# Kernel optimization log

Hardware: AMD Instinct MI355X
Metric: run time of the kernel (lower is better)

Reference implementation:

```python
import jax, jax.numpy as jnp
import numpy as np

IN_DIM, HID, OUT_DIM = 128, 24, 4096
B, K = 16384, 256

def setup_inputs() -> dict:
    key = jax.random.key(0)
    ks = jax.random.split(key, 8)
    x = jax.random.normal(ks[0], (B, IN_DIM), dtype=jnp.float32)
    possible_moves = jax.random.randint(ks[1], (B, K), 0, OUT_DIM)
    s1 = 1.0 / np.sqrt(IN_DIM)
    s2 = 1.0 / np.sqrt(HID)
    W1 = jax.random.uniform(ks[2], (IN_DIM, HID), jnp.float32, -s1, s1)
    b1 = jax.random.uniform(ks[3], (HID,), jnp.float32, -s1, s1)
    W2 = jax.random.uniform(ks[4], (HID, HID), jnp.float32, -s2, s2)
    b2 = jax.random.uniform(ks[5], (HID,), jnp.float32, -s2, s2)
    W3 = jax.random.uniform(ks[6], (HID, OUT_DIM), jnp.float32, -s2, s2)
    b3 = jax.random.uniform(ks[7], (OUT_DIM,), jnp.float32, -s2, s2)
    return {"x": x, "possible_moves": possible_moves,
            "W1": W1, "b1": b1, "W2": W2, "b2": b2, "W3": W3, "b3": b3}

def reference(x, possible_moves, W1, b1, W2, b2, W3, b3):
    # small MLP: 128 -> 24 -> 24 -> 4096
    h = jax.nn.relu(x @ W1 + b1)
    h = jax.nn.relu(h @ W2 + b2)
    logits = h @ W3 + b3                     # [B, OUT_DIM]
    # per-row legal-move mask via vectorized scatter (duplicates just re-set 1)
    Bn = logits.shape[0]
    rows = jnp.arange(Bn)[:, None]           # [B, 1] broadcasts over K
    mask = jnp.zeros_like(logits).at[rows, possible_moves].set(1.0)
    # faithful to original: multiply (not -inf) then softmax over full dim
    filtered = logits * mask
    return jax.nn.softmax(filtered, axis=1)
```

## Files before the change

### kernel.cpp

```cpp
#include <hip/hip_runtime.h>
#include <hip/hip_bf16.h>

#define IN_DIM 128
#define HID 24
#define OUT_DIM 4096
#define NB 16384
#define KMOV 256

#define TR_BLOCKS 384
#define MLP_BLOCKS (NB / 8)

__global__ __launch_bounds__(256) void kprep(const float* __restrict__ x,
                                             const float* __restrict__ W1,
                                             const float* __restrict__ b1,
                                             const float* __restrict__ W2,
                                             const float* __restrict__ b2,
                                             const float* __restrict__ W3,
                                             float* __restrict__ W3T,
                                             float* __restrict__ h2out) {
    __shared__ float W1s[IN_DIM * HID];
    __shared__ float W2s[HID * HID];
    __shared__ float b1s[HID], b2s[HID];
    __shared__ float xs[8][IN_DIM];

    int bid = blockIdx.x;
    int t = threadIdx.x;

    if (bid < TR_BLOCKS) {
        int i = bid * 256 + t;
        int c = i / HID;
        int k = i - c * HID;
        W3T[i] = W3[k * OUT_DIM + c];
        return;
    }

    for (int i = t; i < IN_DIM * HID; i += 256) W1s[i] = W1[i];
    for (int i = t; i < HID * HID; i += 256)    W2s[i] = W2[i];
    if (t < HID) { b1s[t] = b1[t]; b2s[t] = b2[t]; }
    int rbase = (bid - TR_BLOCKS) * 8;
    for (int i = t; i < 8 * IN_DIM; i += 256)
        xs[i >> 7][i & 127] = x[(size_t)rbase * IN_DIM + i];
    __syncthreads();

    int g = t >> 5;
    int j = t & 31;
    int r = rbase + g;

    float h1 = 0.f;
    if (j < HID) {
        h1 = b1s[j];
        #pragma unroll 8
        for (int i = 0; i < IN_DIM; i++) h1 += xs[g][i] * W1s[i * HID + j];
        h1 = fmaxf(h1, 0.f);
    }
    float h2 = (j < HID) ? b2s[j] : 0.f;
    #pragma unroll
    for (int k = 0; k < HID; k++) {
        float hk = __shfl(h1, k, 32);
        if (j < HID) h2 += hk * W2s[k * HID + j];
    }
    if (j < HID) {
        h2 = fmaxf(h2, 0.f);
        h2out[(size_t)r * HID + j] = h2;
    }
}

__global__ __launch_bounds__(256) void kmain(const int* __restrict__ moves,
                                             const float* __restrict__ b3,
                                             const float* __restrict__ W3T,
                                             const float* __restrict__ h2all,
                                             float* __restrict__ out) {
    __shared__ unsigned char claimed[OUT_DIM];
    __shared__ float h2s[HID];
    __shared__ float red[8];

    int r = blockIdx.x;
    int t = threadIdx.x;

    int c = moves[(size_t)r * KMOV + t];
    if (t < HID) h2s[t] = h2all[(size_t)r * HID + t];
    __syncthreads();

    const float4* w = (const float4*)(W3T + c * HID);
    float4 a0 = w[0], a1 = w[1], a2 = w[2], a3 = w[3], a4 = w[4], a5 = w[5];
    float acc = b3[c];
    acc += a0.x*h2s[0] + a0.y*h2s[1] + a0.z*h2s[2]  + a0.w*h2s[3];
    acc += a1.x*h2s[4] + a1.y*h2s[5] + a1.z*h2s[6]  + a1.w*h2s[7];
    acc += a2.x*h2s[8] + a2.y*h2s[9] + a2.z*h2s[10] + a2.w*h2s[11];
    acc += a3.x*h2s[12]+ a3.y*h2s[13]+ a3.z*h2s[14] + a3.w*h2s[15];
    acc += a4.x*h2s[16]+ a4.y*h2s[17]+ a4.z*h2s[18] + a4.w*h2s[19];
    acc += a5.x*h2s[20]+ a5.y*h2s[21]+ a5.z*h2s[22] + a5.w*h2s[23];

    claimed[c] = (unsigned char)t;

    float m = acc;
    #pragma unroll
    for (int off = 32; off > 0; off >>= 1) m = fmaxf(m, __shfl_xor(m, off, 64));
    int wid = t >> 6;
    if ((t & 63) == 0) red[wid] = m;
    __syncthreads();
    float mm = fmaxf(fmaxf(fmaxf(red[0], red[1]), fmaxf(red[2], red[3])), 0.f);

    float e      = __expf(acc - mm);
    float base_e = __expf(-mm);

    float contrib = (claimed[c] == (unsigned char)t) ? (e - base_e) : 0.f;
    float s = contrib;
    #pragma unroll
    for (int off = 32; off > 0; off >>= 1) s += __shfl_xor(s, off, 64);
    if ((t & 63) == 0) red[4 + wid] = s;
    __syncthreads();
    float denom = (float)OUT_DIM * base_e + (red[4] + red[5] + red[6] + red[7]);
    float inv = 1.0f / denom;
    float oc  = base_e * inv;

    float4 ocv = make_float4(oc, oc, oc, oc);
    float4* out4 = (float4*)(out + (size_t)r * OUT_DIM);
    #pragma unroll
    for (int i = 0; i < 4; i++) out4[t + i * 256] = ocv;

    __syncthreads();

    out[(size_t)r * OUT_DIM + c] = e * inv;
}

extern "C" void kernel_launch(void* const* d_in, const int* in_sizes, int n_in,
                              void* d_out, int out_size, void* d_ws, size_t ws_size,
                              hipStream_t stream) {
    const float* x     = (const float*)d_in[0];
    const int*   moves = (const int*)  d_in[1];
    const float* W1    = (const float*)d_in[2];
    const float* b1    = (const float*)d_in[3];
    const float* W2    = (const float*)d_in[4];
    const float* b2    = (const float*)d_in[5];
    const float* W3    = (const float*)d_in[6];
    const float* b3    = (const float*)d_in[7];
    float* out = (float*)d_out;

    float* W3T = (float*)d_ws;
    float* h2  = (float*)((char*)d_ws + OUT_DIM * HID * 4);

    kprep<<<TR_BLOCKS + MLP_BLOCKS, 256, 0, stream>>>(x, W1, b1, W2, b2, W3, W3T, h2);
    kmain<<<NB, 256, 0, stream>>>(moves, b3, W3T, h2, out);
}
```

Baseline: 343.0 us.

## Fuse per-row MLP into main softmax kernel, split W3 transpose into own kernel

Moves the two-layer MLP computation into the per-row main kernel so each block computes its own hidden vector, removing the h2 round trip through global memory. The W3 transpose becomes a tiny separate kernel. In exchange, every one of the 16384 blocks reloads W1 (12 KB) and W2 into shared memory and runs the 128x24 dot products serially on a single wavefront, which adds latency and L2 traffic per block.

```diff
diff --git a/kernel.cpp b/kernel.cpp
--- a/kernel.cpp
+++ b/kernel.cpp
@@ -7,78 +7,61 @@
 #define NB 16384
 #define KMOV 256
 
-#define TR_BLOCKS 384
-#define MLP_BLOCKS (NB / 8)
+__global__ __launch_bounds__(256) void ktr(const float* __restrict__ W3,
+                                           float* __restrict__ W3T) {
+    int i = blockIdx.x * 256 + threadIdx.x;
+    int c = i / HID;
+    int k = i - c * HID;
+    W3T[i] = W3[k * OUT_DIM + c];
+}
 
-__global__ __launch_bounds__(256) void kprep(const float* __restrict__ x,
-                                             const float* __restrict__ W1,
-                                             const float* __restrict__ b1,
-                                             const float* __restrict__ W2,
-                                             const float* __restrict__ b2,
-                                             const float* __restrict__ W3,
-                                             float* __restrict__ W3T,
-                                             float* __restrict__ h2out) {
+__global__ __launch_bounds__(256) void kfused(const float* __restrict__ x,
+                                              const float* __restrict__ W1,
+                                              const float* __restrict__ b1,
+                                              const float* __restrict__ W2,
+                                              const float* __restrict__ b2,
+                                              const float* __restrict__ b3,
+                                              const float* __restrict__ W3T,
+                                              const int* __restrict__ moves,
+                                              float* __restrict__ out) {
     __shared__ float W1s[IN_DIM * HID];
     __shared__ float W2s[HID * HID];
-    __shared__ float b1s[HID], b2s[HID];
-    __shared__ float xs[8][IN_DIM];
-
-    int bid = blockIdx.x;
-    int t = threadIdx.x;
-
-    if (bid < TR_BLOCKS) {
-        int i = bid * 256 + t;
-        int c = i / HID;
-        int k = i - c * HID;
-        W3T[i] = W3[k * OUT_DIM + c];
-        return;
-    }
-
-    for (int i = t; i < IN_DIM * HID; i += 256) W1s[i] = W1[i];
-    for (int i = t; i < HID * HID; i += 256)    W2s[i] = W2[i];
-    if (t < HID) { b1s[t] = b1[t]; b2s[t] = b2[t]; }
-    int rbase = (bid - TR_BLOCKS) * 8;
-    for (int i = t; i < 8 * IN_DIM; i += 256)
-        xs[i >> 7][i & 127] = x[(size_t)rbase * IN_DIM + i];
-    __syncthreads();
-
-    int g = t >> 5;
-    int j = t & 31;
-    int r = rbase + g;
-
-    float h1 = 0.f;
-    if (j < HID) {
-        h1 = b1s[j];
-        #pragma unroll 8
-        for (int i = 0; i < IN_DIM; i++) h1 += xs[g][i] * W1s[i * HID + j];
-        h1 = fmaxf(h1, 0.f);
-    }
-    float h2 = (j < HID) ? b2s[j] : 0.f;
-    #pragma unroll
-    for (int k = 0; k < HID; k++) {
-        float hk = __shfl(h1, k, 32);
-        if (j < HID) h2 += hk * W2s[k * HID + j];
-    }
-    if (j < HID) {
-        h2 = fmaxf(h2, 0.f);
-        h2out[(size_t)r * HID + j] = h2;
-    }
-}
-
-__global__ __launch_bounds__(256) void kmain(const int* __restrict__ moves,
-                                             const float* __restrict__ b3,
-                                             const float* __restrict__ W3T,
-                                             const float* __restrict__ h2all,
-                                             float* __restrict__ out) {
+    __shared__ float xs[IN_DIM];
+    __shared__ float b1s[HID], b2s[HID], h2s[HID];
     __shared__ unsigned char claimed[OUT_DIM];
-    __shared__ float h2s[HID];
     __shared__ float red[8];
 
     int r = blockIdx.x;
     int t = threadIdx.x;
 
+    {
+        float4* W1v = (float4*)W1s;
+        const float4* W1g = (const float4*)W1;
+        #pragma unroll
+        for (int i = 0; i < 3; i++) W1v[t + i * 256] = W1g[t + i * 256];
+        if (t < 144) ((float4*)W2s)[t] = ((const float4*)W2)[t];
+        if (t < IN_DIM) xs[t] = x[(size_t)r * IN_DIM + t];
+        if (t < HID) { b1s[t] = b1[t]; b2s[t] = b2[t]; }
+    }
     int c = moves[(size_t)r * KMOV + t];
-    if (t < HID) h2s[t] = h2all[(size_t)r * HID + t];
+    __syncthreads();
+
+    if (t < 32) {
+        float h1 = 0.f;
+        if (t < HID) {
+            h1 = b1s[t];
+            #pragma unroll 8
+            for (int i = 0; i < IN_DIM; i++) h1 += xs[i] * W1s[i * HID + t];
+            h1 = fmaxf(h1, 0.f);
+        }
+        float h2 = (t < HID) ? b2s[t] : 0.f;
+        #pragma unroll
+        for (int k = 0; k < HID; k++) {
+            float hk = __shfl(h1, k, 32);
+            if (t < HID) h2 += hk * W2s[k * HID + t];
+        }
+        if (t < HID) h2s[t] = fmaxf(h2, 0.f);
+    }
     __syncthreads();
 
     const float4* w = (const float4*)(W3T + c * HID);
@@ -138,8 +121,7 @@
     float* out = (float*)d_out;
 
     float* W3T = (float*)d_ws;
-    float* h2  = (float*)((char*)d_ws + OUT_DIM * HID * 4);
 
-    kprep<<<TR_BLOCKS + MLP_BLOCKS, 256, 0, stream>>>(x, W1, b1, W2, b2, W3, W3T, h2);
-    kmain<<<NB, 256, 0, stream>>>(moves, b3, W3T, h2, out);
+    ktr<<<(OUT_DIM * HID) / 256, 256, 0, stream>>>(W3, W3T);
+    kfused<<<NB, 256, 0, stream>>>(x, W1, b1, W2, b2, b3, W3T, moves, out);
 }
```

Result: slower. 350.3 us (+2.2%).

## Split main kernel into logits and LDS-assembled dense output write kernels

Applied to the files above, without the earlier changes.

The fused kernel is split into two. The first computes the per-move probabilities and the per-row constant and writes them compactly to workspace. The second assembles each full output row in shared memory, constant fill plus scattered moves, and writes it with coalesced float4 stores. This removes the scattered global writes and the double write of move positions, at the cost of an extra launch and a round trip through workspace for the compact probabilities and move indices.

```diff
diff --git a/kernel.cpp b/kernel.cpp
--- a/kernel.cpp
+++ b/kernel.cpp
@@ -9,6 +9,11 @@
 
 #define TR_BLOCKS 384
 #define MLP_BLOCKS (NB / 8)
+
+#define WS_W3T   0
+#define WS_H2    (OUT_DIM * HID * 4)
+#define WS_PROBS (2u * 1024u * 1024u)
+#define WS_OC    (WS_PROBS + NB * KMOV * 4u)
 
 __global__ __launch_bounds__(256) void kprep(const float* __restrict__ x,
                                              const float* __restrict__ W1,
@@ -65,14 +70,15 @@
     }
 }
 
-__global__ __launch_bounds__(256) void kmain(const int* __restrict__ moves,
-                                             const float* __restrict__ b3,
-                                             const float* __restrict__ W3T,
-                                             const float* __restrict__ h2all,
-                                             float* __restrict__ out) {
-    __shared__ unsigned char claimed[OUT_DIM];
+__global__ __launch_bounds__(256) void klogits(const int* __restrict__ moves,
+                                               const float* __restrict__ b3,
+                                               const float* __restrict__ W3T,
+                                               const float* __restrict__ h2all,
+                                               float* __restrict__ probs_c,
+                                               float* __restrict__ ocarr) {
     __shared__ float h2s[HID];
     __shared__ float red[8];
+    __shared__ unsigned char claimed[OUT_DIM];
 
     int r = blockIdx.x;
     int t = threadIdx.x;
@@ -112,16 +118,35 @@
     __syncthreads();
     float denom = (float)OUT_DIM * base_e + (red[4] + red[5] + red[6] + red[7]);
     float inv = 1.0f / denom;
-    float oc  = base_e * inv;
 
+    probs_c[(size_t)r * KMOV + t] = e * inv;
+    if (t == 0) ocarr[r] = base_e * inv;
+}
+
+__global__ __launch_bounds__(256) void kwrite(const int* __restrict__ moves,
+                                              const float* __restrict__ probs_c,
+                                              const float* __restrict__ ocarr,
+                                              float* __restrict__ out) {
+    __shared__ __align__(16) float probs[OUT_DIM];
+
+    int r = blockIdx.x;
+    int t = threadIdx.x;
+
+    int   c  = moves[(size_t)r * KMOV + t];
+    float p  = probs_c[(size_t)r * KMOV + t];
+    float oc = ocarr[r];
+
+    float4* p4 = (float4*)probs;
     float4 ocv = make_float4(oc, oc, oc, oc);
+    #pragma unroll
+    for (int i = 0; i < 4; i++) p4[t + i * 256] = ocv;
+    __syncthreads();
+    probs[c] = p;
+    __syncthreads();
+
     float4* out4 = (float4*)(out + (size_t)r * OUT_DIM);
     #pragma unroll
-    for (int i = 0; i < 4; i++) out4[t + i * 256] = ocv;
-
-    __syncthreads();
-
-    out[(size_t)r * OUT_DIM + c] = e * inv;
+    for (int i = 0; i < 4; i++) out4[t + i * 256] = p4[t + i * 256];
 }
 
 extern "C" void kernel_launch(void* const* d_in, const int* in_sizes, int n_in,
@@ -137,9 +162,13 @@
     const float* b3    = (const float*)d_in[7];
     float* out = (float*)d_out;
 
-    float* W3T = (float*)d_ws;
-    float* h2  = (float*)((char*)d_ws + OUT_DIM * HID * 4);
+    char* ws = (char*)d_ws;
+    float* W3T     = (float*)(ws + WS_W3T);
+    float* h2      = (float*)(ws + WS_H2);
+    float* probs_c = (float*)(ws + WS_PROBS);
+    float* ocarr   = (float*)(ws + WS_OC);
 
     kprep<<<TR_BLOCKS + MLP_BLOCKS, 256, 0, stream>>>(x, W1, b1, W2, b2, W3, W3T, h2);
-    kmain<<<NB, 256, 0, stream>>>(moves, b3, W3T, h2, out);
+    klogits<<<NB, 256, 0, stream>>>(moves, b3, W3T, h2, probs_c, ocarr);
+    kwrite<<<NB, 256, 0, stream>>>(moves, probs_c, ocarr, out);
 }
```

After: 352.9 us. +2.9%, slower.
